# Kernel optimization log

Hardware: AMD Instinct MI355X
Metric: run time of the kernel (lower is better)

## Reference

```python
import jax, jax.numpy as jnp
import numpy as np

B, T_TXT, DIM = 4, 2048, 2048
T_IMG, N_LAT, DIM_VIS = 8, 64, 1024
HEADS, DIM_HEAD = 16, 64
INNER = HEADS * DIM_HEAD
LN_EPS = 1e-5


def setup_inputs() -> dict:
    key = jax.random.key(0)
    ks = jax.random.split(key, 7)
    x = jax.random.normal(ks[0], (B, T_TXT, DIM), dtype=jnp.float32)
    media = jax.random.normal(ks[1], (B, T_IMG, N_LAT, DIM_VIS), dtype=jnp.float32)
    # one media token every T_TXT // T_IMG positions
    media_locations = jnp.zeros((B, T_TXT), dtype=bool)
    media_locations = media_locations.at[:, jnp.arange(T_IMG) * (T_TXT // T_IMG)].set(True)
    norm_w = jnp.ones((DIM,), dtype=jnp.float32)
    norm_b = jnp.zeros((DIM,), dtype=jnp.float32)
    Wq = jax.random.normal(ks[2], (DIM, INNER), dtype=jnp.float32) * (DIM ** -0.5)
    Wkv = jax.random.normal(ks[3], (DIM_VIS, 2 * INNER), dtype=jnp.float32) * (DIM_VIS ** -0.5)
    Wo = jax.random.normal(ks[4], (INNER, DIM), dtype=jnp.float32) * (INNER ** -0.5)
    return {"x": x, "media": media, "norm_w": norm_w, "norm_b": norm_b,
            "Wq": Wq, "Wkv": Wkv, "Wo": Wo, "media_locations": media_locations}


def _layernorm(x, w, b):
    mu = jnp.mean(x, axis=-1, keepdims=True)
    var = jnp.var(x, axis=-1, keepdims=True)
    return (x - mu) * jax.lax.rsqrt(var + LN_EPS) * w + b


def reference(x, media, norm_w, norm_b, Wq, Wkv, Wo, media_locations):
    b, t_txt, _ = x.shape
    _, t_img, n, _ = media.shape
    scale = DIM_HEAD ** -0.5

    xn = _layernorm(x, norm_w, norm_b)
    q = (xn @ Wq).reshape(b, t_txt, HEADS, DIM_HEAD).transpose(0, 2, 1, 3)  # b h i d
    media_f = media.reshape(b, t_img * n, DIM_VIS)
    kv = media_f @ Wkv  # b j 2*inner
    k, v = jnp.split(kv, 2, axis=-1)
    k = k.reshape(b, t_img * n, HEADS, DIM_HEAD).transpose(0, 2, 1, 3)  # b h j d
    v = v.reshape(b, t_img * n, HEADS, DIM_HEAD).transpose(0, 2, 1, 3)

    sim = jnp.einsum('bhid,bhjd->bhij', q * scale, k)  # b h i (t_img*n)

    media_time = jnp.arange(t_img, dtype=jnp.int32) + 1          # (t_img,)
    media_time = jnp.repeat(media_time, n)                        # (t_img*n,)
    text_time = jnp.cumsum(media_locations.astype(jnp.int32), axis=-1)  # (b, t_txt)
    # only_attend_immediate_media -> equality mask
    mask = text_time[:, None, :, None] == media_time[None, None, None, :]
    neg = -jnp.finfo(sim.dtype).max
    sim = jnp.where(mask, sim, neg)

    sim = sim - jax.lax.stop_gradient(jnp.max(sim, axis=-1, keepdims=True))
    attn = jax.nn.softmax(sim, axis=-1)
    # zero attention for text tokens that precede any media
    no_media = (text_time == 0)[:, None, :, None]
    attn = jnp.where(no_media, 0.0, attn)

    out = jnp.einsum('bhij,bhjd->bhid', attn, v)
    out = out.transpose(0, 2, 1, 3).reshape(b, t_txt, INNER)
    return out @ Wo
```

## Files before the change

### kernel.cpp

```cpp
#include <hip/hip_runtime.h>
#include <hip/hip_bf16.h>

#define B_SZ 4
#define T_TXT 2048
#define DIM 2048
#define T_IMG 8
#define N_LAT 64
#define DIM_VIS 1024
#define HEADS 16
#define DIM_HEAD 64
#define INNER 1024
#define T_MED (T_IMG * N_LAT)
#define KV_N (2 * INNER)

typedef _Float16 half8  __attribute__((ext_vector_type(8)));
typedef float    f32x4  __attribute__((ext_vector_type(4)));

#define AS1 __attribute__((address_space(1)))
#define AS3 __attribute__((address_space(3)))

__device__ __forceinline__ void load_lds16(const _Float16* g, _Float16* l)
{
    __builtin_amdgcn_global_load_lds((const AS1 void*)g, (AS3 void*)l, 16, 0, 0);
}

__global__ __launch_bounds__(256)
void prepass(const float* __restrict__ x, const float* __restrict__ gw,
             const float* __restrict__ gb, _Float16* __restrict__ xn,
             const float* __restrict__ media, _Float16* __restrict__ mediaf,
             const float* __restrict__ Wkv, _Float16* __restrict__ wkvT)
{
    __shared__ float red[8];
    __shared__ float tile[32][33];
    const int bid = blockIdx.x;
    const int t = threadIdx.x;

    if (bid < B_SZ * T_TXT) {
        const long row = bid;
        const float* xr = x + row * DIM;
        const int base = t * 8;
        const float4 a = *(const float4*)(xr + base);
        const float4 c = *(const float4*)(xr + base + 4);
        float s  = a.x + a.y + a.z + a.w + c.x + c.y + c.z + c.w;
        float sq = a.x*a.x + a.y*a.y + a.z*a.z + a.w*a.w
                 + c.x*c.x + c.y*c.y + c.z*c.z + c.w*c.w;
#pragma unroll
        for (int off = 32; off; off >>= 1) {
            s  += __shfl_xor(s, off);
            sq += __shfl_xor(sq, off);
        }
        const int wv = t >> 6, ln = t & 63;
        if (ln == 0) { red[wv] = s; red[4 + wv] = sq; }
        __syncthreads();
        s  = red[0] + red[1] + red[2] + red[3];
        sq = red[4] + red[5] + red[6] + red[7];
        const float mean = s * (1.0f / DIM);
        const float var  = sq * (1.0f / DIM) - mean * mean;
        const float rstd = rsqrtf(var + 1e-5f);
        const float4 w0 = *(const float4*)(gw + base);
        const float4 w1 = *(const float4*)(gw + base + 4);
        const float4 b0 = *(const float4*)(gb + base);
        const float4 b1 = *(const float4*)(gb + base + 4);
        half8 o;
        o[0] = (_Float16)((a.x - mean) * rstd * w0.x + b0.x);
        o[1] = (_Float16)((a.y - mean) * rstd * w0.y + b0.y);
        o[2] = (_Float16)((a.z - mean) * rstd * w0.z + b0.z);
        o[3] = (_Float16)((a.w - mean) * rstd * w0.w + b0.w);
        o[4] = (_Float16)((c.x - mean) * rstd * w1.x + b1.x);
        o[5] = (_Float16)((c.y - mean) * rstd * w1.y + b1.y);
        o[6] = (_Float16)((c.z - mean) * rstd * w1.z + b1.z);
        o[7] = (_Float16)((c.w - mean) * rstd * w1.w + b1.w);
        *(half8*)(xn + row * DIM + base) = o;
    } else if (bid < B_SZ * T_TXT + (B_SZ * T_MED * DIM_VIS) / 2048) {
        const long i = ((long)(bid - B_SZ * T_TXT) * 256 + t) * 8;
        const float4 a = *(const float4*)(media + i);
        const float4 c = *(const float4*)(media + i + 4);
        half8 o;
        o[0] = (_Float16)a.x; o[1] = (_Float16)a.y; o[2] = (_Float16)a.z; o[3] = (_Float16)a.w;
        o[4] = (_Float16)c.x; o[5] = (_Float16)c.y; o[6] = (_Float16)c.z; o[7] = (_Float16)c.w;
        *(half8*)(mediaf + i) = o;
    } else {
        const int id = bid - B_SZ * T_TXT - (B_SZ * T_MED * DIM_VIS) / 2048;
        const int n0 = (id & 63) * 32;
        const int k0 = (id >> 6) * 32;
        const int tx = t & 31, ty = t >> 5;
#pragma unroll
        for (int i = 0; i < 32; i += 8)
            tile[ty + i][tx] = Wkv[(long)(k0 + ty + i) * KV_N + n0 + tx];
        __syncthreads();
#pragma unroll
        for (int i = 0; i < 32; i += 8)
            wkvT[(long)(n0 + ty + i) * DIM_VIS + k0 + tx] = (_Float16)tile[tx][ty + i];
    }
}

__global__ __launch_bounds__(256)
void transpose_to_f16(const float* __restrict__ in, _Float16* __restrict__ out,
                      const int K, const int N)
{
    __shared__ float tile[32][33];
    const int k0 = blockIdx.y * 32, n0 = blockIdx.x * 32;
    const int tx = threadIdx.x & 31, ty = threadIdx.x >> 5;
#pragma unroll
    for (int i = 0; i < 32; i += 8)
        tile[ty + i][tx] = in[(long)(k0 + ty + i) * N + n0 + tx];
    __syncthreads();
#pragma unroll
    for (int i = 0; i < 32; i += 8)
        out[(long)(n0 + ty + i) * K + k0 + tx] = (_Float16)tile[tx][ty + i];
}

template<bool C_F16>
__global__ __launch_bounds__(256)
void gemm_tt(const _Float16* __restrict__ A, const _Float16* __restrict__ Bt,
             void* __restrict__ Cp, const int M, const int N, const int K,
             const long aStride, const long cStride)
{
    constexpr int BM = 128, BN = 128, BK = 64;
    __shared__ __align__(16) _Float16 As[BM * BK];
    __shared__ __align__(16) _Float16 Bs[BN * BK];

    const int tid  = threadIdx.x;
    const int lane = tid & 63;
    const int wave = tid >> 6;
    const int wm = wave & 1;
    const int wn = wave >> 1;

    int bx, by;
    {
        const int nB = gridDim.x, mB = gridDim.y;
        const int L = blockIdx.y * nB + blockIdx.x;
        if ((mB & 7) == 0) {
            const int x = L & 7, t = L >> 3;
            const int bandsPer = mB >> 3;
            by = x * bandsPer + (t % bandsPer);
            bx = t / bandsPer;
        } else { bx = blockIdx.x; by = blockIdx.y; }
    }
    const int m0 = by * BM;
    const int n0 = bx * BN;

    const int mrow = lane & 15;
    const int g    = lane >> 4;

    const int srow = wave * 32 + (lane >> 3);
    const int kch  = (((lane & 7) ^ ((lane >> 3) & 7))) * 8;

    const _Float16* Ab = A + blockIdx.z * aStride;

    f32x4 acc[4][4] = {};

    for (int k0 = 0; k0 < K; k0 += BK) {
#pragma unroll
        for (int i = 0; i < 4; ++i) {
            load_lds16(Ab + (long)(m0 + srow + i * 8) * K + k0 + kch,
                       As + (wave * 32 + i * 8) * BK);
            load_lds16(Bt + (long)(n0 + srow + i * 8) * K + k0 + kch,
                       Bs + (wave * 32 + i * 8) * BK);
        }
        __syncthreads();

        half8 afr[4][2], bfr[4][2];
#pragma unroll
        for (int s = 0; s < 2; ++s) {
            const int swz = (((s * 4 + g) ^ (mrow & 7))) * 8;
#pragma unroll
            for (int t = 0; t < 4; ++t) {
                afr[t][s] = *(const half8*)(As + (wm * 64 + t * 16 + mrow) * BK + swz);
                bfr[t][s] = *(const half8*)(Bs + (wn * 64 + t * 16 + mrow) * BK + swz);
            }
        }
#pragma unroll
        for (int ti = 0; ti < 4; ++ti)
#pragma unroll
            for (int tj = 0; tj < 4; ++tj) {
                acc[ti][tj] = __builtin_amdgcn_mfma_f32_16x16x32_f16(
                    afr[ti][0], bfr[tj][0], acc[ti][tj], 0, 0, 0);
                acc[ti][tj] = __builtin_amdgcn_mfma_f32_16x16x32_f16(
                    afr[ti][1], bfr[tj][1], acc[ti][tj], 0, 0, 0);
            }
        __syncthreads();
    }

    const int colb = n0 + wn * 64 + mrow;
    const int rowb = m0 + wm * 64 + (lane >> 4) * 4;
#pragma unroll
    for (int ti = 0; ti < 4; ++ti)
#pragma unroll
        for (int tj = 0; tj < 4; ++tj)
#pragma unroll
            for (int r = 0; r < 4; ++r) {
                const long idx = (long)(rowb + ti * 16 + r) * N + colb + tj * 16;
                if constexpr (C_F16)
                    ((_Float16*)Cp)[blockIdx.z * cStride + idx] = (_Float16)acc[ti][tj][r];
                else
                    ((float*)Cp)[blockIdx.z * cStride + idx] = acc[ti][tj][r];
            }
}

#define GBAR()   do { asm volatile("" ::: "memory"); __builtin_amdgcn_s_barrier(); \
                      asm volatile("" ::: "memory"); } while (0)
#define GLGKM0() do { asm volatile("s_waitcnt lgkmcnt(0)" ::: "memory"); \
                      __builtin_amdgcn_sched_barrier(0); } while (0)
#define GVM(n)   asm volatile("s_waitcnt vmcnt(" #n ")" ::: "memory")

template<bool C_F16>
__global__ __launch_bounds__(512, 2)
void gemm256(const _Float16* __restrict__ A, const _Float16* __restrict__ Bt,
             void* __restrict__ Cp, const int M, const int N, const int K)
{
    __shared__ __align__(16) _Float16 As[2][256 * 64];
    __shared__ __align__(16) _Float16 Bs[2][256 * 64];

    const int tid  = threadIdx.x;
    const int lane = tid & 63;
    const int wave = tid >> 6;
    const int wm   = wave >> 2;
    const int wn   = wave & 3;
    const int c15  = lane & 15;
    const int g    = lane >> 4;

    int bx, by;
    {
        const int nB = gridDim.x, mB = gridDim.y;
        const int L = blockIdx.y * nB + blockIdx.x;
        if ((mB & 7) == 0) {
            const int xcd = L & 7, t2 = L >> 3;
            const int bandsPer = mB >> 3;
            by = xcd * bandsPer + (t2 % bandsPer);
            bx = t2 / bandsPer;
        } else { bx = blockIdx.x; by = blockIdx.y; }
    }
    const int m0 = by * 256, n0 = bx * 256;

    const int srow8 = wave * 8 + (lane >> 3);
    const int sslot = lane & 7;

    auto STAGE_A = [&](const int tt, const int rb) {
        const int row = rb * 64 + srow8;
        load_lds16(A + (long)(m0 + row) * K + tt * 64 + ((sslot ^ (row & 7)) << 3),
                   &As[tt & 1][(rb * 64 + wave * 8) * 64]);
    };
    auto STAGE_B = [&](const int tt, const int rb) {
        const int row = rb * 64 + srow8;
        load_lds16(Bt + (long)(n0 + row) * K + tt * 64 + ((sslot ^ (row & 7)) << 3),
                   &Bs[tt & 1][(rb * 64 + wave * 8) * 64]);
    };

    half8 af[4][2], bf0[2][2], bf1[2][2];
    f32x4 acc[2][2][4][2] = {};

    auto LDA = [&](const int buf, const int sm) {
#pragma unroll
        for (int ti = 0; ti < 4; ++ti) {
            const int row = sm * 128 + wm * 64 + ti * 16 + c15;
#pragma unroll
            for (int s = 0; s < 2; ++s)
                af[ti][s] = *(const half8*)&As[buf][row * 64 + (((s * 4 + g) ^ (row & 7)) << 3)];
        }
    };
    auto LDB = [&](const int buf, const int sn, half8 (&bf)[2][2]) {
#pragma unroll
        for (int tj = 0; tj < 2; ++tj) {
            const int row = sn * 128 + wn * 32 + tj * 16 + c15;
#pragma unroll
            for (int s = 0; s < 2; ++s)
                bf[tj][s] = *(const half8*)&Bs[buf][row * 64 + (((s * 4 + g) ^ (row & 7)) << 3)];
        }
    };
    auto MMA = [&](f32x4 (&aq)[4][2], const half8 (&bf)[2][2]) {
        __builtin_amdgcn_s_setprio(1);
#pragma unroll
        for (int ti = 0; ti < 4; ++ti)
#pragma unroll
            for (int tj = 0; tj < 2; ++tj) {
                aq[ti][tj] = __builtin_amdgcn_mfma_f32_16x16x32_f16(
                    af[ti][0], bf[tj][0], aq[ti][tj], 0, 0, 0);
                aq[ti][tj] = __builtin_amdgcn_mfma_f32_16x16x32_f16(
                    af[ti][1], bf[tj][1], aq[ti][tj], 0, 0, 0);
            }
        __builtin_amdgcn_s_setprio(0);
    };

    STAGE_A(0, 0); STAGE_A(0, 1); STAGE_A(0, 2); STAGE_A(0, 3);
    STAGE_B(0, 0); STAGE_B(0, 1); STAGE_B(0, 2); STAGE_B(0, 3);
    STAGE_A(1, 0); STAGE_A(1, 1);
    STAGE_B(1, 0); STAGE_B(1, 1); STAGE_B(1, 2); STAGE_B(1, 3);
    GVM(6);
    GBAR();

    const int npairs = K >> 7;
    for (int p = 0; p < npairs; ++p) {
        const int t = 2 * p;
        const bool full = (p + 1 < npairs);

        LDA(0, 0); LDB(0, 0, bf0);
        STAGE_A(t + 1, 2); STAGE_A(t + 1, 3);
        GBAR(); GLGKM0();
        MMA(acc[0][0], bf0);
        GBAR();
        LDB(0, 1, bf1);
        if (full) { STAGE_A(t + 2, 0); STAGE_A(t + 2, 1); }
        GBAR(); GLGKM0();
        MMA(acc[0][1], bf1);
        GBAR();
        LDA(0, 1);
        if (full) { STAGE_B(t + 2, 0); STAGE_B(t + 2, 1); }
        GBAR(); GLGKM0();
        MMA(acc[1][1], bf1);
        GBAR();
        if (full) { STAGE_B(t + 2, 2); STAGE_B(t + 2, 3); }
        GBAR();
        MMA(acc[1][0], bf0);
        if (full) { GVM(6); } else { GVM(0); }
        GBAR();
        LDA(1, 0); LDB(1, 0, bf0);
        if (full) { STAGE_A(t + 2, 2); STAGE_A(t + 2, 3); }
        GBAR(); GLGKM0();
        MMA(acc[0][0], bf0);
        GBAR();
        LDB(1, 1, bf1);
        if (full) { STAGE_A(t + 3, 0); STAGE_A(t + 3, 1); }
        GBAR(); GLGKM0();
        MMA(acc[0][1], bf1);
        GBAR();
        LDA(1, 1);
        if (full) { STAGE_B(t + 3, 0); STAGE_B(t + 3, 1); }
        GBAR(); GLGKM0();
        MMA(acc[1][1], bf1);
        GBAR();
        if (full) { STAGE_B(t + 3, 2); STAGE_B(t + 3, 3); }
        GBAR();
        MMA(acc[1][0], bf0);
        if (full) { GVM(6); }
        GBAR();
    }

    const int colb = n0 + wn * 32 + c15;
    const int rowb = m0 + wm * 64 + g * 4;
#pragma unroll
    for (int sm = 0; sm < 2; ++sm)
#pragma unroll
        for (int sn = 0; sn < 2; ++sn)
#pragma unroll
            for (int ti = 0; ti < 4; ++ti)
#pragma unroll
                for (int tj = 0; tj < 2; ++tj)
#pragma unroll
                    for (int r = 0; r < 4; ++r) {
                        const long idx = (long)(rowb + sm * 128 + ti * 16 + r) * N
                                       + colb + sn * 128 + tj * 16;
                        if constexpr (C_F16)
                            ((_Float16*)Cp)[idx] = (_Float16)acc[sm][sn][ti][tj][r];
                        else
                            ((float*)Cp)[idx] = acc[sm][sn][ti][tj][r];
                    }
}

__global__ __launch_bounds__(256)
void attn_mfma(const _Float16* __restrict__ qg, const _Float16* __restrict__ kv,
               _Float16* __restrict__ attn)
{
    constexpr int LP = 72;
    __shared__ __align__(16) _Float16 Ks[64 * LP];
    __shared__ __align__(16) _Float16 Vt[64 * LP];
    __shared__ __align__(16) _Float16 Ps[4 * 64 * LP];

    const int s = blockIdx.x;
    const int h = blockIdx.y;
    const int b = blockIdx.z;
    const int tid  = threadIdx.x;
    const int lane = tid & 63;
    const int w    = tid >> 6;
    const int c15  = lane & 15;
    const int g    = lane >> 4;

    const long kvbase = ((long)(b * T_MED + s * N_LAT)) * KV_N + h * DIM_HEAD;

#pragma unroll
    for (int it = 0; it < 2; ++it) {
        const int id = it * 256 + tid;
        const int key = id >> 3, c = id & 7;
        *(half8*)&Ks[key * LP + c * 8] =
            *(const half8*)(kv + kvbase + (long)key * KV_N + c * 8);
    }
#pragma unroll
    for (int it = 0; it < 2; ++it) {
        const int id = it * 256 + tid;
        const int key = id >> 3, c = id & 7;
        const half8 v = *(const half8*)(kv + kvbase + INNER + (long)key * KV_N + c * 8);
#pragma unroll
        for (int j = 0; j < 8; ++j)
            Vt[(c * 8 + j) * LP + key] = v[j];
    }
    __syncthreads();

    const long q0 = ((long)(b * T_TXT + s * 256 + w * 64)) * INNER + h * DIM_HEAD;
    half8 qf[4][2];
#pragma unroll
    for (int tm = 0; tm < 4; ++tm)
#pragma unroll
        for (int ks = 0; ks < 2; ++ks)
            qf[tm][ks] = *(const half8*)(qg + q0 + (long)(tm * 16 + c15) * INNER + ks * 32 + g * 8);

    f32x4 acc[4][4] = {};
#pragma unroll
    for (int tn = 0; tn < 4; ++tn) {
        const half8 kf0 = *(const half8*)&Ks[(tn * 16 + c15) * LP + g * 8];
        const half8 kf1 = *(const half8*)&Ks[(tn * 16 + c15) * LP + 32 + g * 8];
#pragma unroll
        for (int tm = 0; tm < 4; ++tm) {
            acc[tm][tn] = __builtin_amdgcn_mfma_f32_16x16x32_f16(qf[tm][0], kf0, acc[tm][tn], 0, 0, 0);
            acc[tm][tn] = __builtin_amdgcn_mfma_f32_16x16x32_f16(qf[tm][1], kf1, acc[tm][tn], 0, 0, 0);
        }
    }

    constexpr float sc = 0.125f;
    _Float16* Pw = Ps + w * (64 * LP);
#pragma unroll
    for (int tm = 0; tm < 4; ++tm)
#pragma unroll
        for (int r = 0; r < 4; ++r) {
            float m = fmaxf(fmaxf(acc[tm][0][r], acc[tm][1][r]),
                            fmaxf(acc[tm][2][r], acc[tm][3][r]));
#pragma unroll
            for (int off = 1; off < 16; off <<= 1) m = fmaxf(m, __shfl_xor(m, off));
            float e0 = __expf((acc[tm][0][r] - m) * sc);
            float e1 = __expf((acc[tm][1][r] - m) * sc);
            float e2 = __expf((acc[tm][2][r] - m) * sc);
            float e3 = __expf((acc[tm][3][r] - m) * sc);
            float sum = e0 + e1 + e2 + e3;
#pragma unroll
            for (int off = 1; off < 16; off <<= 1) sum += __shfl_xor(sum, off);
            const float inv = 1.0f / sum;
            const int row = tm * 16 + g * 4 + r;
            Pw[row * LP +  0 + c15] = (_Float16)(e0 * inv);
            Pw[row * LP + 16 + c15] = (_Float16)(e1 * inv);
            Pw[row * LP + 32 + c15] = (_Float16)(e2 * inv);
            Pw[row * LP + 48 + c15] = (_Float16)(e3 * inv);
        }
    __syncthreads();

    f32x4 o[4][4] = {};
#pragma unroll
    for (int ks = 0; ks < 2; ++ks) {
        half8 pf[4];
#pragma unroll
        for (int tm = 0; tm < 4; ++tm)
            pf[tm] = *(const half8*)&Pw[(tm * 16 + c15) * LP + ks * 32 + g * 8];
#pragma unroll
        for (int tn = 0; tn < 4; ++tn) {
            const half8 vf = *(const half8*)&Vt[(tn * 16 + c15) * LP + ks * 32 + g * 8];
#pragma unroll
            for (int tm = 0; tm < 4; ++tm)
                o[tm][tn] = __builtin_amdgcn_mfma_f32_16x16x32_f16(pf[tm], vf, o[tm][tn], 0, 0, 0);
        }
    }

    const long obase = ((long)(b * T_TXT + s * 256 + w * 64)) * INNER + h * DIM_HEAD;
#pragma unroll
    for (int tm = 0; tm < 4; ++tm)
#pragma unroll
        for (int tn = 0; tn < 4; ++tn)
#pragma unroll
            for (int r = 0; r < 4; ++r)
                attn[obase + (long)(tm * 16 + g * 4 + r) * INNER + tn * 16 + c15] =
                    (_Float16)o[tm][tn][r];
}

extern "C" void kernel_launch(void* const* d_in, const int* in_sizes, int n_in,
                              void* d_out, int out_size, void* d_ws, size_t ws_size,
                              hipStream_t stream)
{
    (void)in_sizes; (void)n_in; (void)out_size; (void)ws_size;
    const float* x      = (const float*)d_in[0];
    const float* media  = (const float*)d_in[1];
    const float* norm_w = (const float*)d_in[2];
    const float* norm_b = (const float*)d_in[3];
    const float* Wq     = (const float*)d_in[4];
    const float* Wkv    = (const float*)d_in[5];
    const float* Wo     = (const float*)d_in[6];

    char* ws = (char*)d_ws;
    _Float16* xn     = (_Float16*)ws;
    _Float16* attn   = (_Float16*)ws;
    _Float16* qbuf   = (_Float16*)(ws + (32ull << 20));
    _Float16* mediaf = (_Float16*)(ws + (32ull << 20));
    _Float16* kvb    = (_Float16*)(ws + (48ull << 20));
    _Float16* wslot  = (_Float16*)(ws + (56ull << 20));
    float* out = (float*)d_out;

    prepass<<<dim3(B_SZ * T_TXT + (B_SZ * T_MED * DIM_VIS) / 2048 + (KV_N / 32) * (DIM_VIS / 32)),
              dim3(256), 0, stream>>>(x, norm_w, norm_b, xn, media, mediaf, Wkv, wslot);

    gemm_tt<true><<<dim3(KV_N / 128, T_MED / 128, B_SZ), dim3(256), 0, stream>>>(
        mediaf, wslot, kvb, T_MED, KV_N, DIM_VIS,
        (long)T_MED * DIM_VIS, (long)T_MED * KV_N);

    transpose_to_f16<<<dim3(INNER / 32, DIM / 32), dim3(256), 0, stream>>>(
        Wq, wslot, DIM, INNER);

    gemm_tt<true><<<dim3(INNER / 128, (B_SZ * T_TXT) / 128, 1), dim3(256), 0, stream>>>(
        xn, wslot, qbuf, B_SZ * T_TXT, INNER, DIM, 0, 0);

    attn_mfma<<<dim3(T_IMG, HEADS, B_SZ), dim3(256), 0, stream>>>(qbuf, kvb, attn);

    transpose_to_f16<<<dim3(DIM / 32, INNER / 32), dim3(256), 0, stream>>>(
        Wo, wslot, INNER, DIM);

    gemm256<false><<<dim3(DIM / 256, (B_SZ * T_TXT) / 256), dim3(512), 0, stream>>>(
        attn, wslot, out, B_SZ * T_TXT, DIM, INNER);
}
```

Measured before the change: 272.9 us.

## Add 256x128 pipelined MFMA GEMM for Q projection and flatten KV GEMM batch

Adds a new 512-thread GEMM kernel with 256x128 tiles, double-buffered direct-to-LDS loads and interleaved stage/compute phases, and uses it for the Q projection (8192x1024x2048) in place of the 128x128 gemm_tt. The KV projection is also launched as one flattened 2048-row GEMM instead of a batched z-grid, since the weights are shared across the batch. The larger tiles aim to improve operand reuse and MFMA throughput. The cost is fewer blocks for the Q GEMM (256), which may hurt occupancy and wave balance.

```diff
diff --git a/kernel.cpp b/kernel.cpp
--- a/kernel.cpp
+++ b/kernel.cpp
@@ -23,6 +23,12 @@
 {
     __builtin_amdgcn_global_load_lds((const AS1 void*)g, (AS3 void*)l, 16, 0, 0);
 }
+
+#define GBAR()   do { asm volatile("" ::: "memory"); __builtin_amdgcn_s_barrier(); \
+                      asm volatile("" ::: "memory"); } while (0)
+#define GLGKM0() do { asm volatile("s_waitcnt lgkmcnt(0)" ::: "memory"); \
+                      __builtin_amdgcn_sched_barrier(0); } while (0)
+#define GVM(n)   asm volatile("s_waitcnt vmcnt(" #n ")" ::: "memory")
 
 __global__ __launch_bounds__(256)
 void prepass(const float* __restrict__ x, const float* __restrict__ gw,
@@ -198,25 +204,19 @@
             }
 }
 
-#define GBAR()   do { asm volatile("" ::: "memory"); __builtin_amdgcn_s_barrier(); \
-                      asm volatile("" ::: "memory"); } while (0)
-#define GLGKM0() do { asm volatile("s_waitcnt lgkmcnt(0)" ::: "memory"); \
-                      __builtin_amdgcn_sched_barrier(0); } while (0)
-#define GVM(n)   asm volatile("s_waitcnt vmcnt(" #n ")" ::: "memory")
-
 template<bool C_F16>
 __global__ __launch_bounds__(512, 2)
-void gemm256(const _Float16* __restrict__ A, const _Float16* __restrict__ Bt,
-             void* __restrict__ Cp, const int M, const int N, const int K)
+void gemm_n128(const _Float16* __restrict__ A, const _Float16* __restrict__ Bt,
+               void* __restrict__ Cp, const int M, const int N, const int K)
 {
     __shared__ __align__(16) _Float16 As[2][256 * 64];
-    __shared__ __align__(16) _Float16 Bs[2][256 * 64];
+    __shared__ __align__(16) _Float16 Bs[2][128 * 64];
 
     const int tid  = threadIdx.x;
     const int lane = tid & 63;
     const int wave = tid >> 6;
-    const int wm   = wave >> 2;
-    const int wn   = wave & 3;
+    const int wm   = wave >> 1;
+    const int wn   = wave & 1;
     const int c15  = lane & 15;
     const int g    = lane >> 4;
 
@@ -231,6 +231,133 @@
             bx = t2 / bandsPer;
         } else { bx = blockIdx.x; by = blockIdx.y; }
     }
+    const int m0 = by * 256, n0 = bx * 128;
+
+    const int srow8 = wave * 8 + (lane >> 3);
+    const int sslot = lane & 7;
+
+    auto STAGE_A = [&](const int tt, const int rb) {
+        const int row = rb * 64 + srow8;
+        load_lds16(A + (long)(m0 + row) * K + tt * 64 + ((sslot ^ (row & 7)) << 3),
+                   &As[tt & 1][(rb * 64 + wave * 8) * 64]);
+    };
+    auto STAGE_B = [&](const int tt, const int rb) {
+        const int row = rb * 64 + srow8;
+        load_lds16(Bt + (long)(n0 + row) * K + tt * 64 + ((sslot ^ (row & 7)) << 3),
+                   &Bs[tt & 1][(rb * 64 + wave * 8) * 64]);
+    };
+
+    half8 af[2][2], bf[4][2];
+    f32x4 acc[4][4] = {};
+
+    auto LDA = [&](const int buf, const int h) {
+#pragma unroll
+        for (int i = 0; i < 2; ++i) {
+            const int row = wm * 64 + (h * 2 + i) * 16 + c15;
+#pragma unroll
+            for (int s = 0; s < 2; ++s)
+                af[i][s] = *(const half8*)&As[buf][row * 64 + (((s * 4 + g) ^ (row & 7)) << 3)];
+        }
+    };
+    auto LDB = [&](const int buf) {
+#pragma unroll
+        for (int tj = 0; tj < 4; ++tj) {
+            const int row = wn * 64 + tj * 16 + c15;
+#pragma unroll
+            for (int s = 0; s < 2; ++s)
+                bf[tj][s] = *(const half8*)&Bs[buf][row * 64 + (((s * 4 + g) ^ (row & 7)) << 3)];
+        }
+    };
+    auto MMA = [&](f32x4 (&a0)[4], f32x4 (&a1)[4]) {
+        __builtin_amdgcn_s_setprio(1);
+#pragma unroll
+        for (int tj = 0; tj < 4; ++tj) {
+            a0[tj] = __builtin_amdgcn_mfma_f32_16x16x32_f16(af[0][0], bf[tj][0], a0[tj], 0, 0, 0);
+            a0[tj] = __builtin_amdgcn_mfma_f32_16x16x32_f16(af[0][1], bf[tj][1], a0[tj], 0, 0, 0);
+            a1[tj] = __builtin_amdgcn_mfma_f32_16x16x32_f16(af[1][0], bf[tj][0], a1[tj], 0, 0, 0);
+            a1[tj] = __builtin_amdgcn_mfma_f32_16x16x32_f16(af[1][1], bf[tj][1], a1[tj], 0, 0, 0);
+        }
+        __builtin_amdgcn_s_setprio(0);
+    };
+
+    STAGE_A(0, 0); STAGE_A(0, 1); STAGE_A(0, 2); STAGE_A(0, 3);
+    STAGE_B(0, 0); STAGE_B(0, 1);
+    STAGE_B(1, 0); STAGE_B(1, 1);
+    GVM(2);
+    GBAR();
+
+    const int np = K >> 7;
+    for (int p = 0; p < np; ++p) {
+        const int t = 2 * p;
+        const bool s2 = (p + 1 < np);
+
+        LDA(0, 0); LDB(0);
+        STAGE_A(t + 1, 0); STAGE_A(t + 1, 1); STAGE_A(t + 1, 2); STAGE_A(t + 1, 3);
+        GBAR(); GLGKM0();
+        MMA(acc[0], acc[1]);
+        GBAR();
+        LDA(0, 1);
+        if (s2) { STAGE_B(t + 2, 0); STAGE_B(t + 2, 1); }
+        GBAR(); GLGKM0();
+        MMA(acc[2], acc[3]);
+        if (s2) { GVM(2); } else { GVM(0); }
+        GBAR();
+        LDA(1, 0); LDB(1);
+        if (s2) { STAGE_A(t + 2, 0); STAGE_A(t + 2, 1); STAGE_A(t + 2, 2); STAGE_A(t + 2, 3); }
+        GBAR(); GLGKM0();
+        MMA(acc[0], acc[1]);
+        GBAR();
+        LDA(1, 1);
+        if (s2) { STAGE_B(t + 3, 0); STAGE_B(t + 3, 1); }
+        GBAR(); GLGKM0();
+        MMA(acc[2], acc[3]);
+        if (s2) { GVM(2); }
+        GBAR();
+    }
+
+    const int colb = n0 + wn * 64 + c15;
+    const int rowb = m0 + wm * 64 + g * 4;
+#pragma unroll
+    for (int ti = 0; ti < 4; ++ti)
+#pragma unroll
+        for (int tj = 0; tj < 4; ++tj)
+#pragma unroll
+            for (int r = 0; r < 4; ++r) {
+                const long idx = (long)(rowb + ti * 16 + r) * N + colb + tj * 16;
+                if constexpr (C_F16)
+                    ((_Float16*)Cp)[idx] = (_Float16)acc[ti][tj][r];
+                else
+                    ((float*)Cp)[idx] = acc[ti][tj][r];
+            }
+}
+
+template<bool C_F16>
+__global__ __launch_bounds__(512, 2)
+void gemm256(const _Float16* __restrict__ A, const _Float16* __restrict__ Bt,
+             void* __restrict__ Cp, const int M, const int N, const int K)
+{
+    __shared__ __align__(16) _Float16 As[2][256 * 64];
+    __shared__ __align__(16) _Float16 Bs[2][256 * 64];
+
+    const int tid  = threadIdx.x;
+    const int lane = tid & 63;
+    const int wave = tid >> 6;
+    const int wm   = wave >> 2;
+    const int wn   = wave & 3;
+    const int c15  = lane & 15;
+    const int g    = lane >> 4;
+
+    int bx, by;
+    {
+        const int nB = gridDim.x, mB = gridDim.y;
+        const int L = blockIdx.y * nB + blockIdx.x;
+        if ((mB & 7) == 0) {
+            const int xcd = L & 7, t2 = L >> 3;
+            const int bandsPer = mB >> 3;
+            by = xcd * bandsPer + (t2 % bandsPer);
+            bx = t2 / bandsPer;
+        } else { bx = blockIdx.x; by = blockIdx.y; }
+    }
     const int m0 = by * 256, n0 = bx * 256;
 
     const int srow8 = wave * 8 + (lane >> 3);
@@ -493,15 +620,14 @@
     prepass<<<dim3(B_SZ * T_TXT + (B_SZ * T_MED * DIM_VIS) / 2048 + (KV_N / 32) * (DIM_VIS / 32)),
               dim3(256), 0, stream>>>(x, norm_w, norm_b, xn, media, mediaf, Wkv, wslot);
 
-    gemm_tt<true><<<dim3(KV_N / 128, T_MED / 128, B_SZ), dim3(256), 0, stream>>>(
-        mediaf, wslot, kvb, T_MED, KV_N, DIM_VIS,
-        (long)T_MED * DIM_VIS, (long)T_MED * KV_N);
+    gemm_tt<true><<<dim3(KV_N / 128, (B_SZ * T_MED) / 128, 1), dim3(256), 0, stream>>>(
+        mediaf, wslot, kvb, B_SZ * T_MED, KV_N, DIM_VIS, 0, 0);
 
     transpose_to_f16<<<dim3(INNER / 32, DIM / 32), dim3(256), 0, stream>>>(
         Wq, wslot, DIM, INNER);
 
-    gemm_tt<true><<<dim3(INNER / 128, (B_SZ * T_TXT) / 128, 1), dim3(256), 0, stream>>>(
-        xn, wslot, qbuf, B_SZ * T_TXT, INNER, DIM, 0, 0);
+    gemm_n128<true><<<dim3(INNER / 128, (B_SZ * T_TXT) / 256), dim3(512), 0, stream>>>(
+        xn, wslot, qbuf, B_SZ * T_TXT, INNER, DIM);
 
     attn_mfma<<<dim3(T_IMG, HEADS, B_SZ), dim3(256), 0, stream>>>(qbuf, kvb, attn);
 
```

Result: no change. 271.4 us (-0.5%).
